# Optimization experiments

Measured on AMD Instinct MI355X. Metric: run time of the kernel, lower is better.

Reference implementation:

```python
import jax, jax.numpy as jnp
import numpy as np

B, T, D = 1, 1024, 2048
F_DIM = 1408
E = 8
TOPK = 2


def setup_inputs() -> dict:
    key = jax.random.key(0)
    ks = jax.random.split(key, 5)
    x = jax.random.normal(ks[0], (B, T, D), dtype=jnp.float32)
    # torch nn.Linear weight layout: [out_features, in_features]
    gate_w = jax.random.normal(ks[1], (E, D), dtype=jnp.float32) * 0.02
    gate_proj = jax.random.normal(ks[2], (E, F_DIM, D), dtype=jnp.float32) * 0.02
    up_proj = jax.random.normal(ks[3], (E, F_DIM, D), dtype=jnp.float32) * 0.02
    down_proj = jax.random.normal(ks[4], (E, D, F_DIM), dtype=jnp.float32) * 0.02
    return {"x": x, "gate_w": gate_w, "gate_proj": gate_proj,
            "up_proj": up_proj, "down_proj": down_proj}


def reference(x, gate_w, gate_proj, up_proj, down_proj):
    b, t, d = x.shape
    x_flat = x.reshape(-1, d)                                  # [N, D]
    n = x_flat.shape[0]
    # Router: top-k logits then softmax over the selected k.
    router_logits = x_flat @ gate_w.T                          # [N, E]
    top_w, sel = jax.lax.top_k(router_logits, TOPK)            # [N, K]
    top_w = jax.nn.softmax(top_w, axis=-1)                     # [N, K]
    # Scatter routing weights into dense per-token expert weights [N, E].
    tok_ids = jnp.arange(n)[:, None]
    tw = jnp.zeros((n, E), dtype=x.dtype).at[tok_ids, sel].add(top_w)
    # Dense expert compute (mathematically identical: unselected experts get
    # zero combine weight). SwiGLU per expert.
    g = jnp.einsum('nd,efd->enf', x_flat, gate_proj)           # [E, N, F]
    u = jnp.einsum('nd,efd->enf', x_flat, up_proj)             # [E, N, F]
    h = jax.nn.silu(g) * u                                     # [E, N, F]
    eo = jnp.einsum('enf,edf->end', h, down_proj)              # [E, N, D]
    out = jnp.einsum('end,ne->nd', eo, tw)                     # [N, D]
    return out.reshape(b, t, d)
```

## Files before the change

kernel.cpp:

```cpp
#include <hip/hip_runtime.h>
#include <hip/hip_bf16.h>
#include <stdint.h>

typedef __attribute__((ext_vector_type(8))) short short8;
typedef __attribute__((ext_vector_type(4))) float f32x4;
typedef unsigned int u32;
typedef unsigned short u16;

static constexpr int N_TOK = 1024;
static constexpr int DDIM = 2048;
static constexpr int FDIM = 1408;
static constexpr int NEXP = 8;
static constexpr int MAXROWS = 3072;
static constexpr int NT128 = 24;

static constexpr size_t O_META   = 0;
static constexpr size_t O_TE128  = 256;
static constexpr size_t O_TR128  = 384;
static constexpr size_t O_ROWTOK = 768;
static constexpr size_t O_TOKROWS= O_ROWTOK + (size_t)MAXROWS * 4;
static constexpr size_t O_SEL    = O_TOKROWS + 2048 * 4;
static constexpr size_t O_W      = O_SEL + 2048 * 4;
static constexpr size_t O_XBF    = (O_W + 2048 * 4 + 255) & ~(size_t)255;
static constexpr size_t O_H      = O_XBF + (size_t)(N_TOK + 1) * DDIM * 2;
static constexpr size_t O_EO     = O_H + (size_t)MAXROWS * FDIM * 2;

static __device__ __forceinline__ u16 f2bf(float f) {
    return __builtin_bit_cast(u16, __float2bfloat16(f));
}
static __device__ __forceinline__ float bf2f(u16 s) {
    u32 u = ((u32)s) << 16;
    return __builtin_bit_cast(float, u);
}
static __device__ __forceinline__ u32 pack2(float a, float b) {
    return (u32)f2bf(a) | ((u32)f2bf(b) << 16);
}
static __device__ __forceinline__ void gload16(const void* g, void* l) {
    __builtin_amdgcn_global_load_lds(
        (const __attribute__((address_space(1))) void*)g,
        (__attribute__((address_space(3))) void*)l, 16, 0, 0);
}

__global__ __launch_bounds__(256) void xcast_kernel(
    const float* __restrict__ x, u16* __restrict__ xbf)
{
    const long idx = ((long)blockIdx.x * 256 + threadIdx.x) * 8;
    uint4 v = {0u, 0u, 0u, 0u};
    if (idx < (long)N_TOK * DDIM) {
        const float4 f0 = *(const float4*)(x + idx);
        const float4 f1 = *(const float4*)(x + idx + 4);
        v.x = pack2(f0.x, f0.y); v.y = pack2(f0.z, f0.w);
        v.z = pack2(f1.x, f1.y); v.w = pack2(f1.z, f1.w);
    }
    *(uint4*)(xbf + idx) = v;
}

__global__ __launch_bounds__(256) void router_kernel(
    const float* __restrict__ x, const float* __restrict__ gw,
    int* __restrict__ sel, float* __restrict__ wout)
{
    __shared__ float xs[DDIM];
    __shared__ float lg[NEXP];
    const int tok = blockIdx.x;
    const float* xr = x + (size_t)tok * DDIM;
    for (int i = threadIdx.x; i < DDIM / 4; i += 256)
        ((float4*)xs)[i] = ((const float4*)xr)[i];
    __syncthreads();
    const int wid = threadIdx.x >> 6, lane = threadIdx.x & 63;
    for (int i = 0; i < 2; i++) {
        const int e = wid * 2 + i;
        const float* g = gw + (size_t)e * DDIM;
        float s = 0.f;
        for (int k = lane; k < DDIM; k += 64) s += xs[k] * g[k];
        for (int off = 32; off > 0; off >>= 1) s += __shfl_down(s, off);
        if (lane == 0) lg[e] = s;
    }
    __syncthreads();
    if (threadIdx.x == 0) {
        int i1 = 0;
        for (int e = 1; e < NEXP; e++) if (lg[e] > lg[i1]) i1 = e;
        int i2 = -1;
        for (int e = 0; e < NEXP; e++) {
            if (e == i1) continue;
            if (i2 < 0 || lg[e] > lg[i2]) i2 = e;
        }
        const float e2 = __expf(lg[i2] - lg[i1]);
        const float w1 = 1.f / (1.f + e2);
        sel[tok * 2] = i1; sel[tok * 2 + 1] = i2;
        wout[tok * 2] = w1; wout[tok * 2 + 1] = e2 * w1;
    }
}

__global__ __launch_bounds__(512) void build_kernel(
    const int* __restrict__ sel,
    int* __restrict__ meta, int* __restrict__ te128, int* __restrict__ tr128,
    int* __restrict__ row_tok, int* __restrict__ tok_rows)
{
    __shared__ int s0[N_TOK], s1[N_TOK];
    __shared__ u16 p0[N_TOK], p1[N_TOK];
    __shared__ int counts[NEXP], offs[NEXP];
    for (int i = threadIdx.x; i < N_TOK; i += 512) {
        s0[i] = sel[i * 2]; s1[i] = sel[i * 2 + 1];
    }
    __syncthreads();
    const int e = threadIdx.x >> 6, lane = threadIdx.x & 63;
    int base = 0;
    for (int c = 0; c < N_TOK / 64; c++) {
        const int tk = c * 64 + lane;
        const int slot = (s0[tk] == e) ? 0 : ((s1[tk] == e) ? 1 : -1);
        const unsigned long long m = __ballot(slot >= 0);
        const int pre = __popcll(m & ((1ull << lane) - 1ull));
        if (slot == 0) p0[tk] = (u16)(base + pre);
        else if (slot == 1) p1[tk] = (u16)(base + pre);
        base += __popcll(m);
    }
    if (lane == 0) counts[e] = base;
    __syncthreads();
    if (threadIdx.x == 0) {
        int off = 0, n128 = 0;
        for (int qq = 0; qq < NEXP; qq++) {
            offs[qq] = off;
            const int pc = (counts[qq] + 127) & ~127;
            for (int i = 0; i < pc / 128; i++) { te128[n128] = qq; tr128[n128] = off + i * 128; n128++; }
            off += pc;
        }
        meta[0] = n128; meta[1] = off;
    }
    __syncthreads();
    const int off = offs[e];
    for (int c = 0; c < N_TOK / 64; c++) {
        const int tk = c * 64 + lane;
        const int slot = (s0[tk] == e) ? 0 : ((s1[tk] == e) ? 1 : -1);
        if (slot >= 0) {
            const int row = off + (slot ? p1[tk] : p0[tk]);
            row_tok[row] = tk;
            tok_rows[tk * 2 + slot] = row;
        }
    }
    const int cnt = counts[e];
    const int pc = (cnt + 127) & ~127;
    for (int p = cnt + lane; p < pc; p += 64) row_tok[off + p] = -1;
}

__global__ __launch_bounds__(512, 6) void mlp1_kernel(
    const u16* __restrict__ xbf,
    const float* __restrict__ gp, const float* __restrict__ upw,
    u16* __restrict__ h,
    const int* __restrict__ meta, const int* __restrict__ te128,
    const int* __restrict__ tr128, const int* __restrict__ row_tok)
{
    const int tile = blockIdx.y;
    const int nb = blockIdx.x;
    if (tile >= meta[0]) return;
    const int n0 = nb * 32;
    const int e = te128[tile];
    const int r0g = tr128[tile];

    __shared__ __align__(16) u16 As[2][128 * 64];
    __shared__ __align__(16) u16 Bs0[2][32 * 64];
    __shared__ __align__(16) u16 Bs1[2][32 * 64];

    const int t = threadIdx.x;
    const int wid = t >> 6, lane = t & 63;
    const int lr = lane & 15, lhi = lane >> 4;

    const u16* asrc[2];
    int aldsoff[2];
    #pragma unroll
    for (int j = 0; j < 2; j++) {
        const int row = (wid * 2 + j) * 8 + (lane >> 3);
        const int gran = (lane & 7) ^ (row & 7);
        const int tok = row_tok[r0g + row];
        asrc[j] = xbf + (size_t)(tok < 0 ? N_TOK : tok) * DDIM + gran * 8;
        aldsoff[j] = (wid * 2 + j) * 512;
    }

    const int rb = t >> 4, c4 = t & 15;
    const float* brow0 = gp  + (size_t)e * FDIM * DDIM + (size_t)(n0 + rb) * DDIM + c4 * 4;
    const float* brow1 = upw + (size_t)e * FDIM * DDIM + (size_t)(n0 + rb) * DDIM + c4 * 4;
    const int sOffB = rb * 64 + (((c4 >> 1) ^ (rb & 7)) * 8) + (c4 & 1) * 4;

    const int wm = (wid >> 1) * 32, wn = (wid & 1) * 16;

    f32x4 acc0[2], acc1[2];
    acc0[0] = acc0[1] = acc1[0] = acc1[1] = f32x4{0.f, 0.f, 0.f, 0.f};
    float4 pb0, pb1;

    auto STAGEA = [&](int bsel, int k0) {
        #pragma unroll
        for (int j = 0; j < 2; j++)
            gload16(asrc[j] + k0, &As[bsel][aldsoff[j]]);
    };
    auto LOADB = [&](int k0) {
        pb0 = *(const float4*)(brow0 + k0);
        pb1 = *(const float4*)(brow1 + k0);
    };
    auto STOREB = [&](int bsel) {
        uint2 v0; v0.x = pack2(pb0.x, pb0.y); v0.y = pack2(pb0.z, pb0.w);
        *(uint2*)(&Bs0[bsel][sOffB]) = v0;
        uint2 v1; v1.x = pack2(pb1.x, pb1.y); v1.y = pack2(pb1.z, pb1.w);
        *(uint2*)(&Bs1[bsel][sOffB]) = v1;
    };
    auto COMPUTE = [&](int bsel) {
        #pragma unroll
        for (int ks = 0; ks < 2; ks++) {
            short8 a[2], b0, b1;
            #pragma unroll
            for (int m = 0; m < 2; m++) {
                const int rowa = wm + m * 16 + lr;
                const int gr = (ks * 4 + lhi) ^ (rowa & 7);
                a[m] = *(const short8*)(&As[bsel][rowa * 64 + gr * 8]);
            }
            {
                const int rowb = wn + lr;
                const int gr = (ks * 4 + lhi) ^ (rowb & 7);
                b0 = *(const short8*)(&Bs0[bsel][rowb * 64 + gr * 8]);
                b1 = *(const short8*)(&Bs1[bsel][rowb * 64 + gr * 8]);
            }
            #pragma unroll
            for (int m = 0; m < 2; m++) {
                acc0[m] = __builtin_amdgcn_mfma_f32_16x16x32_bf16(a[m], b0, acc0[m], 0, 0, 0);
                acc1[m] = __builtin_amdgcn_mfma_f32_16x16x32_bf16(a[m], b1, acc1[m], 0, 0, 0);
            }
        }
    };

    constexpr int NT = DDIM / 64;
    STAGEA(0, 0); LOADB(0); STOREB(0);
    __syncthreads();
    for (int kt = 0; kt < NT; kt++) {
        const int cur = kt & 1;
        const bool more = (kt + 1 < NT);
        if (more) { STAGEA(cur ^ 1, (kt + 1) * 64); LOADB((kt + 1) * 64); }
        COMPUTE(cur);
        if (more) {
            STOREB(cur ^ 1);
            __syncthreads();
        }
    }

    #pragma unroll
    for (int m = 0; m < 2; m++) {
        const int col = n0 + wn + lr;
        #pragma unroll
        for (int j = 0; j < 4; j++) {
            const int row = r0g + wm + m * 16 + lhi * 4 + j;
            const float g = acc0[m][j], u = acc1[m][j];
            const float hv = g / (1.f + __expf(-g)) * u;
            h[(size_t)row * FDIM + col] = f2bf(hv);
        }
    }
}

__global__ __launch_bounds__(512, 6) void down_kernel(
    const u16* __restrict__ h, const float* __restrict__ dp,
    u16* __restrict__ eo,
    const int* __restrict__ meta, const int* __restrict__ te128,
    const int* __restrict__ tr128)
{
    const int tile = blockIdx.y;
    const int nb = blockIdx.x;
    if (tile >= meta[0]) return;
    const int n0 = nb * 32;
    const int e = te128[tile];
    const int r0g = tr128[tile];

    __shared__ __align__(16) u16 As[2][128 * 64];
    __shared__ __align__(16) u16 Bs[2][32 * 64];

    const int t = threadIdx.x;
    const int wid = t >> 6, lane = t & 63;
    const int lr = lane & 15, lhi = lane >> 4;

    const u16* asrc[2];
    int aldsoff[2];
    #pragma unroll
    for (int j = 0; j < 2; j++) {
        const int row = (wid * 2 + j) * 8 + (lane >> 3);
        const int gran = (lane & 7) ^ (row & 7);
        asrc[j] = h + (size_t)(r0g + row) * FDIM + gran * 8;
        aldsoff[j] = (wid * 2 + j) * 512;
    }

    const int rb = t >> 4, c4 = t & 15;
    const float* brow = dp + (size_t)e * DDIM * FDIM + (size_t)(n0 + rb) * FDIM + c4 * 4;
    const int sOffB = rb * 64 + (((c4 >> 1) ^ (rb & 7)) * 8) + (c4 & 1) * 4;

    const int wm = (wid >> 1) * 32, wn = (wid & 1) * 16;

    f32x4 acc[2];
    acc[0] = acc[1] = f32x4{0.f, 0.f, 0.f, 0.f};
    float4 pb;

    auto STAGEA = [&](int bsel, int k0) {
        #pragma unroll
        for (int j = 0; j < 2; j++)
            gload16(asrc[j] + k0, &As[bsel][aldsoff[j]]);
    };
    auto LOADB = [&](int k0) { pb = *(const float4*)(brow + k0); };
    auto STOREB = [&](int bsel) {
        uint2 v; v.x = pack2(pb.x, pb.y); v.y = pack2(pb.z, pb.w);
        *(uint2*)(&Bs[bsel][sOffB]) = v;
    };
    auto COMPUTE = [&](int bsel) {
        #pragma unroll
        for (int ks = 0; ks < 2; ks++) {
            short8 a[2], b;
            #pragma unroll
            for (int m = 0; m < 2; m++) {
                const int rowa = wm + m * 16 + lr;
                const int gr = (ks * 4 + lhi) ^ (rowa & 7);
                a[m] = *(const short8*)(&As[bsel][rowa * 64 + gr * 8]);
            }
            {
                const int rowb = wn + lr;
                const int gr = (ks * 4 + lhi) ^ (rowb & 7);
                b = *(const short8*)(&Bs[bsel][rowb * 64 + gr * 8]);
            }
            #pragma unroll
            for (int m = 0; m < 2; m++)
                acc[m] = __builtin_amdgcn_mfma_f32_16x16x32_bf16(a[m], b, acc[m], 0, 0, 0);
        }
    };

    constexpr int NT = FDIM / 64;
    STAGEA(0, 0); LOADB(0); STOREB(0);
    __syncthreads();
    for (int kt = 0; kt < NT; kt++) {
        const int cur = kt & 1;
        const bool more = (kt + 1 < NT);
        if (more) { STAGEA(cur ^ 1, (kt + 1) * 64); LOADB((kt + 1) * 64); }
        COMPUTE(cur);
        if (more) {
            STOREB(cur ^ 1);
            __syncthreads();
        }
    }

    #pragma unroll
    for (int m = 0; m < 2; m++) {
        const int col = n0 + wn + lr;
        #pragma unroll
        for (int j = 0; j < 4; j++) {
            const int row = r0g + wm + m * 16 + lhi * 4 + j;
            eo[(size_t)row * DDIM + col] = f2bf(acc[m][j]);
        }
    }
}

__global__ __launch_bounds__(256) void combine_kernel(
    const u16* __restrict__ eo, const int* __restrict__ tok_rows,
    const float* __restrict__ w, float* __restrict__ out)
{
    const int tok = blockIdx.x;
    const int r1 = tok_rows[tok * 2], r2 = tok_rows[tok * 2 + 1];
    const float w1 = w[tok * 2], w2 = w[tok * 2 + 1];
    const int d = threadIdx.x * 8;
    const uint4 a = *(const uint4*)(eo + (size_t)r1 * DDIM + d);
    const uint4 b = *(const uint4*)(eo + (size_t)r2 * DDIM + d);
    const u32 av[4] = {a.x, a.y, a.z, a.w};
    const u32 bv[4] = {b.x, b.y, b.z, b.w};
    float4 o0, o1;
    float* op[8] = {&o0.x, &o0.y, &o0.z, &o0.w, &o1.x, &o1.y, &o1.z, &o1.w};
    #pragma unroll
    for (int i = 0; i < 4; i++) {
        *op[2 * i]     = w1 * bf2f((u16)(av[i] & 0xffff)) + w2 * bf2f((u16)(bv[i] & 0xffff));
        *op[2 * i + 1] = w1 * bf2f((u16)(av[i] >> 16))    + w2 * bf2f((u16)(bv[i] >> 16));
    }
    float4* po = (float4*)(out + (size_t)tok * DDIM + d);
    po[0] = o0; po[1] = o1;
}

extern "C" void kernel_launch(void* const* d_in, const int* in_sizes, int n_in,
                              void* d_out, int out_size, void* d_ws, size_t ws_size,
                              hipStream_t stream) {
    const float* x  = (const float*)d_in[0];
    const float* gw = (const float*)d_in[1];
    const float* gp = (const float*)d_in[2];
    const float* up = (const float*)d_in[3];
    const float* dp = (const float*)d_in[4];
    float* out = (float*)d_out;
    char* ws = (char*)d_ws;

    int*   meta     = (int*)(ws + O_META);
    int*   te128    = (int*)(ws + O_TE128);
    int*   tr128    = (int*)(ws + O_TR128);
    int*   row_tok  = (int*)(ws + O_ROWTOK);
    int*   tok_rows = (int*)(ws + O_TOKROWS);
    int*   sel      = (int*)(ws + O_SEL);
    float* w        = (float*)(ws + O_W);
    u16*   xbf      = (u16*)(ws + O_XBF);
    u16*   h        = (u16*)(ws + O_H);
    u16*   eo       = (u16*)(ws + O_EO);

    xcast_kernel<<<((N_TOK + 1) * DDIM) / (256 * 8), 256, 0, stream>>>(x, xbf);
    router_kernel<<<N_TOK, 256, 0, stream>>>(x, gw, sel, w);
    build_kernel<<<1, 512, 0, stream>>>(sel, meta, te128, tr128, row_tok, tok_rows);
    mlp1_kernel<<<dim3(FDIM / 32, NT128), 512, 0, stream>>>(
        xbf, gp, up, h, meta, te128, tr128, row_tok);
    down_kernel<<<dim3(DDIM / 32, NT128), 512, 0, stream>>>(
        h, dp, eo, meta, te128, tr128);
    combine_kernel<<<N_TOK, 256, 0, stream>>>(eo, tok_rows, w, out);
}
```

Measured before the change: 195.1 us.

## Unroll GEMM K-loop by two with ping-pong B register prefetch and MFMA priority

Both the gate/up and down expert GEMM kernels now unroll the K loop by two. They use two sets of B-tile registers (P/Q), so the fp32 weight loads for a tile are issued one compute phase earlier. The bf16 pack and LDS store happen before the MFMA phase rather than after it. COMPUTE is also wrapped in s_setprio(1)/s_setprio(0) to favour waves issuing MFMAs. The aim is to hide global-load latency for the fp32 weights and cut stalls at the barriers, at the cost of more live registers, which could reduce occupancy.

```diff
diff --git a/kernel.cpp b/kernel.cpp
--- a/kernel.cpp
+++ b/kernel.cpp
@@ -184,24 +184,35 @@
 
     f32x4 acc0[2], acc1[2];
     acc0[0] = acc0[1] = acc1[0] = acc1[1] = f32x4{0.f, 0.f, 0.f, 0.f};
-    float4 pb0, pb1;
+    float4 pb0P, pb1P, pb0Q, pb1Q;
 
     auto STAGEA = [&](int bsel, int k0) {
         #pragma unroll
         for (int j = 0; j < 2; j++)
             gload16(asrc[j] + k0, &As[bsel][aldsoff[j]]);
     };
-    auto LOADB = [&](int k0) {
-        pb0 = *(const float4*)(brow0 + k0);
-        pb1 = *(const float4*)(brow1 + k0);
-    };
-    auto STOREB = [&](int bsel) {
-        uint2 v0; v0.x = pack2(pb0.x, pb0.y); v0.y = pack2(pb0.z, pb0.w);
+    auto LOADB_P = [&](int k0) {
+        pb0P = *(const float4*)(brow0 + k0);
+        pb1P = *(const float4*)(brow1 + k0);
+    };
+    auto LOADB_Q = [&](int k0) {
+        pb0Q = *(const float4*)(brow0 + k0);
+        pb1Q = *(const float4*)(brow1 + k0);
+    };
+    auto STOREB_P = [&](int bsel) {
+        uint2 v0; v0.x = pack2(pb0P.x, pb0P.y); v0.y = pack2(pb0P.z, pb0P.w);
         *(uint2*)(&Bs0[bsel][sOffB]) = v0;
-        uint2 v1; v1.x = pack2(pb1.x, pb1.y); v1.y = pack2(pb1.z, pb1.w);
+        uint2 v1; v1.x = pack2(pb1P.x, pb1P.y); v1.y = pack2(pb1P.z, pb1P.w);
         *(uint2*)(&Bs1[bsel][sOffB]) = v1;
     };
+    auto STOREB_Q = [&](int bsel) {
+        uint2 v0; v0.x = pack2(pb0Q.x, pb0Q.y); v0.y = pack2(pb0Q.z, pb0Q.w);
+        *(uint2*)(&Bs0[bsel][sOffB]) = v0;
+        uint2 v1; v1.x = pack2(pb1Q.x, pb1Q.y); v1.y = pack2(pb1Q.z, pb1Q.w);
+        *(uint2*)(&Bs1[bsel][sOffB]) = v1;
+    };
     auto COMPUTE = [&](int bsel) {
+        __builtin_amdgcn_s_setprio(1);
         #pragma unroll
         for (int ks = 0; ks < 2; ks++) {
             short8 a[2], b0, b1;
@@ -223,20 +234,25 @@
                 acc1[m] = __builtin_amdgcn_mfma_f32_16x16x32_bf16(a[m], b1, acc1[m], 0, 0, 0);
             }
         }
+        __builtin_amdgcn_s_setprio(0);
     };
 
     constexpr int NT = DDIM / 64;
-    STAGEA(0, 0); LOADB(0); STOREB(0);
-    __syncthreads();
-    for (int kt = 0; kt < NT; kt++) {
-        const int cur = kt & 1;
-        const bool more = (kt + 1 < NT);
-        if (more) { STAGEA(cur ^ 1, (kt + 1) * 64); LOADB((kt + 1) * 64); }
-        COMPUTE(cur);
-        if (more) {
-            STOREB(cur ^ 1);
-            __syncthreads();
-        }
+    STAGEA(0, 0);
+    LOADB_P(0);
+    STOREB_P(0);
+    LOADB_Q(64);
+    for (int kt = 0; kt < NT; kt += 2) {
+        __syncthreads();
+        if (kt + 1 < NT) STAGEA(1, (kt + 1) * 64);
+        if (kt + 2 < NT) LOADB_P((kt + 2) * 64);
+        if (kt + 1 < NT) STOREB_Q(1);
+        COMPUTE(0);
+        __syncthreads();
+        if (kt + 2 < NT) STAGEA(0, (kt + 2) * 64);
+        if (kt + 3 < NT) LOADB_Q((kt + 3) * 64);
+        if (kt + 2 < NT) STOREB_P(0);
+        COMPUTE(1);
     }
 
     #pragma unroll
@@ -290,19 +306,25 @@
 
     f32x4 acc[2];
     acc[0] = acc[1] = f32x4{0.f, 0.f, 0.f, 0.f};
-    float4 pb;
+    float4 pbP, pbQ;
 
     auto STAGEA = [&](int bsel, int k0) {
         #pragma unroll
         for (int j = 0; j < 2; j++)
             gload16(asrc[j] + k0, &As[bsel][aldsoff[j]]);
     };
-    auto LOADB = [&](int k0) { pb = *(const float4*)(brow + k0); };
-    auto STOREB = [&](int bsel) {
-        uint2 v; v.x = pack2(pb.x, pb.y); v.y = pack2(pb.z, pb.w);
+    auto LOADB_P = [&](int k0) { pbP = *(const float4*)(brow + k0); };
+    auto LOADB_Q = [&](int k0) { pbQ = *(const float4*)(brow + k0); };
+    auto STOREB_P = [&](int bsel) {
+        uint2 v; v.x = pack2(pbP.x, pbP.y); v.y = pack2(pbP.z, pbP.w);
         *(uint2*)(&Bs[bsel][sOffB]) = v;
     };
+    auto STOREB_Q = [&](int bsel) {
+        uint2 v; v.x = pack2(pbQ.x, pbQ.y); v.y = pack2(pbQ.z, pbQ.w);
+        *(uint2*)(&Bs[bsel][sOffB]) = v;
+    };
     auto COMPUTE = [&](int bsel) {
+        __builtin_amdgcn_s_setprio(1);
         #pragma unroll
         for (int ks = 0; ks < 2; ks++) {
             short8 a[2], b;
@@ -321,20 +343,25 @@
             for (int m = 0; m < 2; m++)
                 acc[m] = __builtin_amdgcn_mfma_f32_16x16x32_bf16(a[m], b, acc[m], 0, 0, 0);
         }
+        __builtin_amdgcn_s_setprio(0);
     };
 
     constexpr int NT = FDIM / 64;
-    STAGEA(0, 0); LOADB(0); STOREB(0);
-    __syncthreads();
-    for (int kt = 0; kt < NT; kt++) {
-        const int cur = kt & 1;
-        const bool more = (kt + 1 < NT);
-        if (more) { STAGEA(cur ^ 1, (kt + 1) * 64); LOADB((kt + 1) * 64); }
-        COMPUTE(cur);
-        if (more) {
-            STOREB(cur ^ 1);
-            __syncthreads();
-        }
+    STAGEA(0, 0);
+    LOADB_P(0);
+    STOREB_P(0);
+    LOADB_Q(64);
+    for (int kt = 0; kt < NT; kt += 2) {
+        __syncthreads();
+        if (kt + 1 < NT) STAGEA(1, (kt + 1) * 64);
+        if (kt + 2 < NT) LOADB_P((kt + 2) * 64);
+        if (kt + 1 < NT) STOREB_Q(1);
+        COMPUTE(0);
+        __syncthreads();
+        if (kt + 2 < NT) STAGEA(0, (kt + 2) * 64);
+        if (kt + 3 < NT) LOADB_Q((kt + 3) * 64);
+        if (kt + 2 < NT) STOREB_P(0);
+        COMPUTE(1);
     }
 
     #pragma unroll
```

Measured after the change: 289.1 us. 48.2% more time.
